# Optimization experiments

Measured on AMD Instinct MI355X. Metric: run time of the kernel, lower is better.

Reference implementation:

```python
import jax, jax.numpy as jnp
import numpy as np

DIM = 128
CODEBOOK_SIZE = 1024

def setup_inputs() -> dict:
    key = jax.random.key(0)
    k1, k2 = jax.random.split(key)
    x = jax.random.normal(k1, (16, 4096, DIM), dtype=jnp.float32)
    embed = jax.random.normal(k2, (CODEBOOK_SIZE, DIM), dtype=jnp.float32)
    return {"x": x, "embed": embed}

def reference(x, embed):
    # preprocess: flatten leading dims -> (N, d)
    shape = x.shape
    flat = x.reshape(-1, shape[-1])  # (N, d)
    x_sq = jnp.sum(flat * flat, axis=1, keepdims=True)        # (N, 1)
    e_sq = jnp.sum(embed * embed, axis=1)[None, :]            # (1, K)
    dist = -(x_sq - 2.0 * (flat @ embed.T) + e_sq)            # (N, K)
    embed_ind = jnp.argmax(dist, axis=-1)                     # (N,)
    embed_ind = embed_ind.reshape(shape[:-1])                 # (...,)
    quantize = jnp.take(embed, embed_ind, axis=0)             # (..., d)
    return (quantize, embed_ind)
```

## Files before the change

kernel.cpp:

```cpp
#include <hip/hip_runtime.h>

#define NRD   65536
#define DIMD  128
#define KCB   1024
#define RPB   64
#define NBLK  (NRD / RPB)
#define MARGIN 0.40f

typedef float f32x4 __attribute__((ext_vector_type(4)));
typedef short short8 __attribute__((ext_vector_type(8)));

#define WS_ESQ   0
#define WS_CNT   4096
#define WS_LIST  8192
#define WS_B     270336
#define WS_ET2   532480
#define WS_NEED  1056768

__device__ inline unsigned short f2bf(float f) {
    unsigned u = __float_as_uint(f);
    u += 0x7FFFu + ((u >> 16) & 1u);
    return (unsigned short)(u >> 16);
}

__device__ inline short8 pack_h(float4 a, float4 b) {
    short8 r;
    r[0]=(short)f2bf(a.x); r[1]=(short)f2bf(a.y); r[2]=(short)f2bf(a.z); r[3]=(short)f2bf(a.w);
    r[4]=(short)f2bf(b.x); r[5]=(short)f2bf(b.y); r[6]=(short)f2bf(b.z); r[7]=(short)f2bf(b.w);
    return r;
}

__global__ __launch_bounds__(256, 2) void prep_kernel(const float* __restrict__ embed,
                                                      float* __restrict__ esq,
                                                      float4* __restrict__ bblob,
                                                      float4* __restrict__ et4,
                                                      int* __restrict__ cnt,
                                                      int doTrans) {
    __shared__ float tile[64][129];
    const int t = threadIdx.x;
    {
        int gw   = blockIdx.x * 4 + (t >> 6);
        int lane = t & 63;
        const float* row = embed + (size_t)gw * DIMD;
        float a = row[lane], b = row[lane + 64];
        float v = a * a + b * b;
        #pragma unroll
        for (int off = 32; off >= 1; off >>= 1) v += __shfl_xor(v, off, 64);
        if (lane == 0) esq[gw] = v;
    }
    if (blockIdx.x < 64) {
        int tid  = blockIdx.x * 256 + t;
        int lane = tid & 63;
        int ctg  = (tid >> 6) & 15;
        int ksh  = (tid >> 10) & 1;
        int s    = tid >> 11;
        int chunk = s >> 1, kh = s & 1;
        int ks = kh * 2 + ksh;
        int l15 = lane & 15, l4 = lane >> 4;
        int code = chunk * 256 + ctg * 16 + l15;
        int d0   = ks * 32 + l4 * 8;
        const float4* e4 = (const float4*)(embed + (size_t)code * DIMD + d0);
        short8 v = pack_h(e4[0], e4[1]);
        bblob[tid] = *(float4*)&v;
    }
    if (doTrans && blockIdx.x >= 64 && blockIdx.x < 80) {
        const int c0 = (blockIdx.x - 64) * 64;
        #pragma unroll
        for (int i = 0; i < 8; ++i) {
            int u = t + i * 256;
            int row = u >> 5, col4 = u & 31;
            float4 v = ((const float4*)embed)[(size_t)(c0 + row) * 32 + col4];
            tile[row][col4 * 4 + 0] = v.x;
            tile[row][col4 * 4 + 1] = v.y;
            tile[row][col4 * 4 + 2] = v.z;
            tile[row][col4 * 4 + 3] = v.w;
        }
        __syncthreads();
        #pragma unroll
        for (int i = 0; i < 8; ++i) {
            int u = t + i * 256;
            int d = u >> 4, off = u & 15;
            float4 v;
            v.x = tile[off * 4 + 0][d];
            v.y = tile[off * 4 + 1][d];
            v.z = tile[off * 4 + 2][d];
            v.w = tile[off * 4 + 3][d];
            et4[(size_t)d * 256 + (c0 >> 2) + off] = v;
        }
    }
    if (blockIdx.x == 128 && t == 0) cnt[0] = 0;
}

__global__ __launch_bounds__(512, 4) void vq_mfma(const float* __restrict__ x,
                                                  const float* __restrict__ embed,
                                                  const float* __restrict__ esq,
                                                  const float4* __restrict__ bblob,
                                                  float* __restrict__ out_q,
                                                  float* __restrict__ out_idx,
                                                  int* __restrict__ cnt,
                                                  int* __restrict__ list) {
    __shared__ __align__(16) short Atrans[4][4][512];
    __shared__ __align__(16) short Bb[32][512];
    __shared__ float rbest[4][RPB];
    __shared__ int   rmeta[4][RPB];
    __shared__ float rb2[4][RPB];

    const int t    = threadIdx.x;
    const int lane = t & 63;
    const int w    = __builtin_amdgcn_readfirstlane(t >> 6);
    const int rg   = w >> 2, cg = w & 3;
    const int l15  = lane & 15, l4 = lane >> 4;
    const int row0 = blockIdx.x * RPB;

    const int ksA = w & 3, jh = w >> 2;
    const float4* xs = (const float4*)(x + (size_t)(row0 + lane) * DIMD + ksA * 32 + jh * 16);
    float4 xv0 = xs[0], xv1 = xs[1], xv2 = xs[2], xv3 = xs[3];

#define GLDS(sv) do {                                                                                   \
    const char* g_ = (const char*)bblob + (size_t)(sv) * 32768 + ((size_t)w * 64 + lane) * 16;          \
    _Pragma("unroll")                                                                                   \
    for (int k_ = 0; k_ < 4; ++k_)                                                                      \
        __builtin_amdgcn_global_load_lds(                                                               \
            (const __attribute__((address_space(1))) unsigned int*)(g_ + k_ * 8192),                    \
            (__attribute__((address_space(3))) unsigned int*)&Bb[k_ * 8 + w][0], 16, 0, 0);             \
} while (0)

    GLDS(0);

    const int rtA = lane >> 4, riA = lane & 15;
    *(short8*)&Atrans[ksA][rtA][((jh * 2 + 0) * 16 + riA) * 8] = pack_h(xv0, xv1);
    *(short8*)&Atrans[ksA][rtA][((jh * 2 + 1) * 16 + riA) * 8] = pack_h(xv2, xv3);
    asm volatile("s_waitcnt lgkmcnt(0)" ::: "memory");
    __builtin_amdgcn_s_barrier();

    short8 ahr[4][2];
    #pragma unroll
    for (int ks = 0; ks < 4; ++ks)
        #pragma unroll
        for (int rt = 0; rt < 2; ++rt)
            ahr[ks][rt] = *(const short8*)&Atrans[ks][rg * 2 + rt][lane * 8];
    asm volatile("s_waitcnt vmcnt(0) lgkmcnt(0)" ::: "memory");
    __builtin_amdgcn_s_barrier();

    f32x4 acc[2][4];
    float best[2][4]; int bidx[2][4]; float b2[2][4];
    #pragma unroll
    for (int i = 0; i < 2; ++i)
        #pragma unroll
        for (int j = 0; j < 4; ++j) { best[i][j] = -1e30f; bidx[i][j] = 0; b2[i][j] = -1e30f; }

    const float* esqp = esq + cg * 64 + l15;
    float eq0 = 0.f, eq1 = 0.f, eq2 = 0.f, eq3 = 0.f;

#define STEP(khv) do {                                                                  \
    const int s_ = c * 2 + khv;                                                         \
    if (khv == 0) {                                                                     \
        eq0 = esqp[c * 256];      eq1 = esqp[c * 256 + 16];                             \
        eq2 = esqp[c * 256 + 32]; eq3 = esqp[c * 256 + 48];                             \
        _Pragma("unroll")                                                               \
        for (int i_ = 0; i_ < 2; ++i_)                                                  \
            _Pragma("unroll")                                                           \
            for (int j_ = 0; j_ < 4; ++j_) acc[i_][j_] = (f32x4){0.f, 0.f, 0.f, 0.f};   \
    }                                                                                   \
    short8 bh_[2][4];                                                                   \
    _Pragma("unroll")                                                                   \
    for (int ksh_ = 0; ksh_ < 2; ++ksh_)                                                \
        _Pragma("unroll")                                                               \
        for (int ct_ = 0; ct_ < 4; ++ct_)                                               \
            bh_[ksh_][ct_] = *(const short8*)&Bb[ksh_ * 16 + cg * 4 + ct_][lane * 8];   \
    asm volatile("s_waitcnt lgkmcnt(0)" ::: "memory");                                  \
    __builtin_amdgcn_s_barrier();                            \
    if (s_ < 7) GLDS(s_ + 1);                                   \
    _Pragma("unroll")                                                                   \
    for (int ksh_ = 0; ksh_ < 2; ++ksh_) {                                              \
        _Pragma("unroll")                                                               \
        for (int ct_ = 0; ct_ < 4; ++ct_) {                                             \
            _Pragma("unroll")                                                           \
            for (int rt_ = 0; rt_ < 2; ++rt_)                                           \
                acc[rt_][ct_] = __builtin_amdgcn_mfma_f32_16x16x32_bf16(ahr[khv * 2 + ksh_][rt_], bh_[ksh_][ct_], acc[rt_][ct_], 0, 0, 0); \
        }                                                                               \
    }                                                                                   \
    if (khv == 1) {                           \
        _Pragma("unroll")                                                               \
        for (int ct_ = 0; ct_ < 4; ++ct_) {                                             \
            int code_ = c * 256 + cg * 64 + ct_ * 16 + l15;                             \
            float eq_ = (ct_ == 0) ? eq0 : (ct_ == 1) ? eq1 : (ct_ == 2) ? eq2 : eq3;   \
            _Pragma("unroll")                                                           \
            for (int rt_ = 0; rt_ < 2; ++rt_)                                           \
                _Pragma("unroll")                                                       \
                for (int r_ = 0; r_ < 4; ++r_) {                                        \
                    float sc_ = 2.0f * acc[rt_][ct_][r_] - eq_;                         \
                    b2[rt_][r_] = fmaxf(b2[rt_][r_], fminf(sc_, best[rt_][r_]));        \
                    if (sc_ > best[rt_][r_]) { best[rt_][r_] = sc_; bidx[rt_][r_] = code_; } \
                }                                                                       \
        }                                                                               \
    }                                                                                   \
    if (s_ < 7) {                                                                       \
        asm volatile("s_waitcnt vmcnt(0)" ::: "memory");          \
        __builtin_amdgcn_s_barrier();                                                   \
    }                                                                                   \
} while (0)

    for (int c = 0; c < 4; ++c) {
        STEP(0); STEP(1);
    }
#undef STEP
#undef GLDS

    #pragma unroll
    for (int rt = 0; rt < 2; ++rt)
        #pragma unroll
        for (int r = 0; r < 4; ++r) {
            float v = best[rt][r]; int i = bidx[rt][r]; float s2 = b2[rt][r];
            #pragma unroll
            for (int off = 1; off < 16; off <<= 1) {
                float ov = __shfl_xor(v, off, 64);
                int   oi = __shfl_xor(i, off, 64);
                float o2 = __shfl_xor(s2, off, 64);
                s2 = fmaxf(fmaxf(s2, o2), fminf(v, ov));
                bool sw = (ov > v) || (ov == v && oi < i);
                if (sw) { v = ov; i = oi; }
            }
            if (l15 == 0) {
                int rl = rg * 32 + rt * 16 + l4 * 4 + r;
                rbest[cg][rl] = v;
                rmeta[cg][rl] = i;
                rb2[cg][rl]   = s2;
            }
        }
    __syncthreads();
    if (t < RPB) {
        float b = rbest[0][t]; int i = rmeta[0][t]; float s2 = rb2[0][t];
        #pragma unroll
        for (int g = 1; g < 4; ++g) {
            float ob = rbest[g][t]; int oi = rmeta[g][t]; float o2 = rb2[g][t];
            s2 = fmaxf(fmaxf(s2, o2), fminf(b, ob));
            bool sw = (ob > b) || (ob == b && oi < i);
            if (sw) { b = ob; i = oi; }
        }
        out_idx[row0 + t] = (float)i;
        if (s2 >= b - MARGIN) { int pos = atomicAdd(cnt, 1); list[pos] = row0 + t; }
        rmeta[0][t] = i;
    }
    __syncthreads();
    {
        int row = t >> 3, part = t & 7;
        int idx = rmeta[0][row];
        const float4* src = (const float4*)(embed + (size_t)idx * DIMD + part * 16);
        float4* dst = (float4*)(out_q + (size_t)(row0 + row) * DIMD + part * 16);
        #pragma unroll
        for (int q = 0; q < 4; ++q) dst[q] = src[q];
    }
}

__global__ __launch_bounds__(256, 2) void trans_kernel(const float* __restrict__ embed,
                                                       float4* __restrict__ et4) {
    __shared__ float tile[64][129];
    const int t = threadIdx.x;
    const int c0 = blockIdx.x * 64;
    #pragma unroll
    for (int i = 0; i < 8; ++i) {
        int u = t + i * 256;
        int row = u >> 5, col4 = u & 31;
        float4 v = ((const float4*)embed)[(size_t)(c0 + row) * 32 + col4];
        tile[row][col4 * 4 + 0] = v.x;
        tile[row][col4 * 4 + 1] = v.y;
        tile[row][col4 * 4 + 2] = v.z;
        tile[row][col4 * 4 + 3] = v.w;
    }
    __syncthreads();
    #pragma unroll
    for (int i = 0; i < 8; ++i) {
        int u = t + i * 256;
        int d = u >> 4, off = u & 15;
        float4 v;
        v.x = tile[off * 4 + 0][d];
        v.y = tile[off * 4 + 1][d];
        v.z = tile[off * 4 + 2][d];
        v.w = tile[off * 4 + 3][d];
        et4[(size_t)d * 256 + (c0 >> 2) + off] = v;
    }
}

__global__ __launch_bounds__(256, 2) void refine_kernel(const float* __restrict__ x,
                                                        const float* __restrict__ embed,
                                                        const float* __restrict__ esq,
                                                        const f32x4* __restrict__ et4,
                                                        float* __restrict__ out_q,
                                                        float* __restrict__ out_idx,
                                                        const int* __restrict__ cnt,
                                                        const int* __restrict__ list) {
    __shared__ float xls[4][4][128];
    const int t = threadIdx.x, lane = t & 63, w = t >> 6;
    const int n = cnt[0];
    const int njobs = (n + 3) >> 2;
    for (int job = blockIdx.x * 4 + w; job < njobs; job += gridDim.x * 4) {
        int rows[4];
        #pragma unroll
        for (int i = 0; i < 4; ++i) {
            int li = job * 4 + i; if (li >= n) li = n - 1;
            rows[i] = list[li];
        }
        float xsq[4];
        #pragma unroll
        for (int i = 0; i < 4; ++i) {
            float2 xv = *(const float2*)(x + (size_t)rows[i] * DIMD + lane * 2);
            xls[w][i][lane * 2]     = xv.x;
            xls[w][i][lane * 2 + 1] = xv.y;
            float s = xv.x * xv.x + xv.y * xv.y;
            #pragma unroll
            for (int off = 32; off >= 1; off >>= 1) s += __shfl_xor(s, off, 64);
            xsq[i] = s;
        }
        f32x4 acc[4][4];
        #pragma unroll
        for (int i = 0; i < 4; ++i)
            #pragma unroll
            for (int g = 0; g < 4; ++g) acc[i][g] = (f32x4){0.f, 0.f, 0.f, 0.f};

        for (int d0 = 0; d0 < 32; ++d0) {
            float4 xd[4];
            #pragma unroll
            for (int i = 0; i < 4; ++i) xd[i] = *(const float4*)&xls[w][i][d0 * 4];
            #pragma unroll
            for (int dd = 0; dd < 4; ++dd) {
                const f32x4* ep = et4 + (size_t)(d0 * 4 + dd) * 256 + lane;
                f32x4 e0 = ep[0], e1 = ep[64], e2 = ep[128], e3 = ep[192];
                #pragma unroll
                for (int i = 0; i < 4; ++i) {
                    float xsc = (dd == 0) ? xd[i].x : (dd == 1) ? xd[i].y
                              : (dd == 2) ? xd[i].z : xd[i].w;
                    acc[i][0] = e0 * xsc + acc[i][0];
                    acc[i][1] = e1 * xsc + acc[i][1];
                    acc[i][2] = e2 * xsc + acc[i][2];
                    acc[i][3] = e3 * xsc + acc[i][3];
                }
            }
        }

        #pragma unroll
        for (int i = 0; i < 4; ++i) {
            float bv = -1e30f; int bi = 0;
            #pragma unroll
            for (int g = 0; g < 4; ++g) {
                float4 eq = *(const float4*)&esq[g * 256 + lane * 4];
                #pragma unroll
                for (int c2 = 0; c2 < 4; ++c2) {
                    float eqv = (c2 == 0) ? eq.x : (c2 == 1) ? eq.y : (c2 == 2) ? eq.z : eq.w;
                    float sc = -(__fadd_rn(__fsub_rn(xsq[i], __fmul_rn(2.0f, acc[i][g][c2])), eqv));
                    int code = g * 256 + lane * 4 + c2;
                    if (sc > bv) { bv = sc; bi = code; }
                }
            }
            #pragma unroll
            for (int off = 32; off >= 1; off >>= 1) {
                float ov = __shfl_xor(bv, off, 64);
                int   oi = __shfl_xor(bi, off, 64);
                if (ov > bv || (ov == bv && oi < bi)) { bv = ov; bi = oi; }
            }
            if (lane == 0) out_idx[rows[i]] = (float)bi;
            if (lane < 32) {
                float4 v = ((const float4*)embed)[(size_t)bi * 32 + lane];
                ((float4*)out_q)[(size_t)rows[i] * 32 + lane] = v;
            }
        }
    }
}

extern "C" void kernel_launch(void* const* d_in, const int* in_sizes, int n_in,
                              void* d_out, int out_size, void* d_ws, size_t ws_size,
                              hipStream_t stream) {
    const float* x     = (const float*)d_in[0];
    const float* embed = (const float*)d_in[1];
    float* out     = (float*)d_out;
    float* out_q   = out;
    float* out_idx = out + (size_t)NRD * DIMD;

    char*  wsb  = (char*)d_ws;
    float* esq  = (float*)(wsb + WS_ESQ);
    int*   cnt  = (int*)(wsb + WS_CNT);
    int*   list = (int*)(wsb + WS_LIST);
    float4* bblob = (float4*)(wsb + WS_B);

    const int fused = (ws_size >= (size_t)WS_NEED) ? 1 : 0;
    f32x4* et4 = fused ? (f32x4*)(wsb + WS_ET2) : (f32x4*)(wsb + WS_B);

    prep_kernel  <<<dim3(256),  dim3(256), 0, stream>>>(embed, esq, bblob, (float4*)et4, cnt, fused);
    vq_mfma      <<<dim3(NBLK), dim3(512), 0, stream>>>(x, embed, esq, bblob, out_q, out_idx, cnt, list);
    if (!fused)
        trans_kernel<<<dim3(16), dim3(256), 0, stream>>>(embed, (float4*)et4);
    refine_kernel<<<dim3(256),  dim3(256), 0, stream>>>(x, embed, esq, et4, out_q, out_idx, cnt, list);
}
```

Baseline: 81.10 us.

## Pipeline codebook loads at half-stage granularity and stage e_sq in LDS

The main loop is restructured so each 32KB codebook stage is loaded as two halves, each prefetched while the other half is being consumed. Waits use vmcnt(2) in place of a full drain, and MFMA sections run at raised s_setprio. The codebook squared norms are copied once into LDS, reusing the A-staging buffer, instead of being read from global memory every chunk. The refine kernel grid is also doubled. The tighter pipeline adds barriers and relies on exact vmcnt accounting; the final iteration issues a load that wraps back to stage 0 and is never used, which is wasted bandwidth.

```diff
diff --git a/kernel.cpp b/kernel.cpp
--- a/kernel.cpp
+++ b/kernel.cpp
@@ -111,21 +111,13 @@
     const int rg   = w >> 2, cg = w & 3;
     const int l15  = lane & 15, l4 = lane >> 4;
     const int row0 = blockIdx.x * RPB;
+    float* esqs    = (float*)&Atrans[0][0][0];
+
+    const float2 ev = *(const float2*)(esq + t * 2);
 
     const int ksA = w & 3, jh = w >> 2;
     const float4* xs = (const float4*)(x + (size_t)(row0 + lane) * DIMD + ksA * 32 + jh * 16);
     float4 xv0 = xs[0], xv1 = xs[1], xv2 = xs[2], xv3 = xs[3];
-
-#define GLDS(sv) do {                                                                                   \
-    const char* g_ = (const char*)bblob + (size_t)(sv) * 32768 + ((size_t)w * 64 + lane) * 16;          \
-    _Pragma("unroll")                                                                                   \
-    for (int k_ = 0; k_ < 4; ++k_)                                                                      \
-        __builtin_amdgcn_global_load_lds(                                                               \
-            (const __attribute__((address_space(1))) unsigned int*)(g_ + k_ * 8192),                    \
-            (__attribute__((address_space(3))) unsigned int*)&Bb[k_ * 8 + w][0], 16, 0, 0);             \
-} while (0)
-
-    GLDS(0);
 
     const int rtA = lane >> 4, riA = lane & 15;
     *(short8*)&Atrans[ksA][rtA][((jh * 2 + 0) * 16 + riA) * 8] = pack_h(xv0, xv1);
@@ -139,8 +131,26 @@
         #pragma unroll
         for (int rt = 0; rt < 2; ++rt)
             ahr[ks][rt] = *(const short8*)&Atrans[ks][rg * 2 + rt][lane * 8];
-    asm volatile("s_waitcnt vmcnt(0) lgkmcnt(0)" ::: "memory");
+    asm volatile("s_waitcnt lgkmcnt(0)" ::: "memory");
     __builtin_amdgcn_s_barrier();
+
+    *(float2*)&esqs[t * 2] = ev;
+    asm volatile("s_waitcnt lgkmcnt(0)" ::: "memory");
+    asm volatile("s_waitcnt vmcnt(0)" ::: "memory");
+
+#define GLDS_HALF(s2, kshv) do {                                                                        \
+    const char* g_ = (const char*)bblob + (size_t)(s2) * 32768 + (size_t)(kshv) * 16384                 \
+                   + ((size_t)w * 64 + lane) * 16;                                                      \
+    __builtin_amdgcn_global_load_lds(                                                                   \
+        (const __attribute__((address_space(1))) unsigned int*)(g_),                                    \
+        (__attribute__((address_space(3))) unsigned int*)&Bb[(kshv) * 16 + w][0], 16, 0, 0);            \
+    __builtin_amdgcn_global_load_lds(                                                                   \
+        (const __attribute__((address_space(1))) unsigned int*)(g_ + 8192),                             \
+        (__attribute__((address_space(3))) unsigned int*)&Bb[(kshv) * 16 + 8 + w][0], 16, 0, 0);        \
+} while (0)
+
+    GLDS_HALF(0, 0);
+    GLDS_HALF(0, 1);
 
     f32x4 acc[2][4];
     float best[2][4]; int bidx[2][4]; float b2[2][4];
@@ -149,38 +159,41 @@
         #pragma unroll
         for (int j = 0; j < 4; ++j) { best[i][j] = -1e30f; bidx[i][j] = 0; b2[i][j] = -1e30f; }
 
-    const float* esqp = esq + cg * 64 + l15;
     float eq0 = 0.f, eq1 = 0.f, eq2 = 0.f, eq3 = 0.f;
 
-#define STEP(khv) do {                                                                  \
-    const int s_ = c * 2 + khv;                                                         \
-    if (khv == 0) {                                                                     \
-        eq0 = esqp[c * 256];      eq1 = esqp[c * 256 + 16];                             \
-        eq2 = esqp[c * 256 + 32]; eq3 = esqp[c * 256 + 48];                             \
+#define HSTEP(khv_, ksh_) do {                                                          \
+    asm volatile("s_waitcnt vmcnt(2)" ::: "memory");                                    \
+    __builtin_amdgcn_s_barrier();                   \
+    short8 bh_[4];                                                                      \
+    _Pragma("unroll")                                                                   \
+    for (int ct_ = 0; ct_ < 4; ++ct_)                                                   \
+        bh_[ct_] = *(const short8*)&Bb[(ksh_) * 16 + cg * 4 + ct_][lane * 8];           \
+    if ((khv_) == 0 && (ksh_) == 0) {                                                   \
+        eq0 = esqs[c * 256 + cg * 64 + l15];                                            \
+        eq1 = esqs[c * 256 + cg * 64 + l15 + 16];                                       \
+        eq2 = esqs[c * 256 + cg * 64 + l15 + 32];                                       \
+        eq3 = esqs[c * 256 + cg * 64 + l15 + 48];                                       \
         _Pragma("unroll")                                                               \
         for (int i_ = 0; i_ < 2; ++i_)                                                  \
             _Pragma("unroll")                                                           \
             for (int j_ = 0; j_ < 4; ++j_) acc[i_][j_] = (f32x4){0.f, 0.f, 0.f, 0.f};   \
     }                                                                                   \
-    short8 bh_[2][4];                                                                   \
+    asm volatile("s_waitcnt lgkmcnt(0)" ::: "memory");                                  \
+    __builtin_amdgcn_s_barrier();               \
+    if ((khv_) == 1 && (ksh_) == 1) {                                                   \
+        if (c < 3) GLDS_HALF(c * 2 + 2, 1);                                             \
+    } else {                                                                            \
+        GLDS_HALF((c * 2 + (khv_) + 1) & 7, (ksh_));      \
+    }                                                                                   \
+    __builtin_amdgcn_s_setprio(1);                                                      \
     _Pragma("unroll")                                                                   \
-    for (int ksh_ = 0; ksh_ < 2; ++ksh_)                                                \
+    for (int ct_ = 0; ct_ < 4; ++ct_)                                                   \
         _Pragma("unroll")                                                               \
-        for (int ct_ = 0; ct_ < 4; ++ct_)                                               \
-            bh_[ksh_][ct_] = *(const short8*)&Bb[ksh_ * 16 + cg * 4 + ct_][lane * 8];   \
-    asm volatile("s_waitcnt lgkmcnt(0)" ::: "memory");                                  \
-    __builtin_amdgcn_s_barrier();                            \
-    if (s_ < 7) GLDS(s_ + 1);                                   \
-    _Pragma("unroll")                                                                   \
-    for (int ksh_ = 0; ksh_ < 2; ++ksh_) {                                              \
-        _Pragma("unroll")                                                               \
-        for (int ct_ = 0; ct_ < 4; ++ct_) {                                             \
-            _Pragma("unroll")                                                           \
-            for (int rt_ = 0; rt_ < 2; ++rt_)                                           \
-                acc[rt_][ct_] = __builtin_amdgcn_mfma_f32_16x16x32_bf16(ahr[khv * 2 + ksh_][rt_], bh_[ksh_][ct_], acc[rt_][ct_], 0, 0, 0); \
-        }                                                                               \
-    }                                                                                   \
-    if (khv == 1) {                           \
+        for (int rt_ = 0; rt_ < 2; ++rt_)                                               \
+            acc[rt_][ct_] = __builtin_amdgcn_mfma_f32_16x16x32_bf16(                    \
+                ahr[(khv_) * 2 + (ksh_)][rt_], bh_[ct_], acc[rt_][ct_], 0, 0, 0);       \
+    __builtin_amdgcn_s_setprio(0);                                                      \
+    if ((khv_) == 1 && (ksh_) == 1) {         \
         _Pragma("unroll")                                                               \
         for (int ct_ = 0; ct_ < 4; ++ct_) {                                             \
             int code_ = c * 256 + cg * 64 + ct_ * 16 + l15;                             \
@@ -195,17 +208,15 @@
                 }                                                                       \
         }                                                                               \
     }                                                                                   \
-    if (s_ < 7) {                                                                       \
-        asm volatile("s_waitcnt vmcnt(0)" ::: "memory");          \
-        __builtin_amdgcn_s_barrier();                                                   \
-    }                                                                                   \
 } while (0)
 
+    #pragma clang loop unroll(disable)
     for (int c = 0; c < 4; ++c) {
-        STEP(0); STEP(1);
-    }
-#undef STEP
-#undef GLDS
+        HSTEP(0, 0); HSTEP(0, 1); HSTEP(1, 0); HSTEP(1, 1);
+    }
+#undef HSTEP
+#undef GLDS_HALF
+    asm volatile("s_waitcnt vmcnt(0)" ::: "memory");
 
     #pragma unroll
     for (int rt = 0; rt < 2; ++rt)
@@ -389,5 +400,5 @@
     vq_mfma      <<<dim3(NBLK), dim3(512), 0, stream>>>(x, embed, esq, bblob, out_q, out_idx, cnt, list);
     if (!fused)
         trans_kernel<<<dim3(16), dim3(256), 0, stream>>>(embed, (float4*)et4);
-    refine_kernel<<<dim3(256),  dim3(256), 0, stream>>>(x, embed, esq, et4, out_q, out_idx, cnt, list);
-}
+    refine_kernel<<<dim3(512),  dim3(256), 0, stream>>>(x, embed, esq, et4, out_q, out_idx, cnt, list);
+}
```

After: 85.05 us. 4.9% more time.
